# Kernel tuning notes

Measured on AMD Instinct MI355X. Metric: run time of the kernel, lower is better.

Reference implementation:

```python
import jax, jax.numpy as jnp
import numpy as np

N_U = 20000; N_I = 20000; D = 256
NNZ = 600000; EGG = 300000; EDD = 300000; B = 8192
DROP = 0.1; LAM2 = 1e-7


def _attention(x, W, a, edges):
    # GAT-style attention over sampled relationship edges (src -> tgt).
    n, d = x.shape
    h = x @ W                                  # [n, d]
    src, tgt = edges[0], edges[1]
    e = jax.nn.leaky_relu((h @ a[:d])[src] + (h @ a[d:])[tgt], 0.2)  # [E]
    m = jax.ops.segment_max(e, tgt, num_segments=n)
    m = jnp.where(jnp.isfinite(m), m, 0.0)
    ex = jnp.exp(e - m[tgt])
    denom = jax.ops.segment_sum(ex, tgt, num_segments=n)             # [n]
    num = jax.ops.segment_sum(ex[:, None] * h[src], tgt, num_segments=n)  # [n, d]
    return num / (denom[:, None] + 1e-9)


def _spmm(rows, cols, vals, x, n_out):
    # sparse [n_out, n_in] @ dense [n_in, d]
    return jax.ops.segment_sum(vals[:, None] * x[cols], rows, num_segments=n_out)


def _mlp(x, W1, b1, W2, b2, W3, b3):
    h = jax.nn.relu(x @ W1 + b1)
    h = jax.nn.relu(h @ W2 + b2)
    return (h @ W3 + b3)[..., 0]


def setup_inputs() -> dict:
    key = jax.random.key(0)
    ks = jax.random.split(key, 24)
    s = 0.02
    inp = {
        'E_g_0': jax.random.normal(ks[0], (N_U, D), jnp.float32) * s,
        'E_d_0': jax.random.normal(ks[1], (N_I, D), jnp.float32) * s,
        'att_W': jax.random.normal(ks[2], (D, D), jnp.float32) * s,
        'att_a': jax.random.normal(ks[3], (2 * D,), jnp.float32) * s,
        'att1_W': jax.random.normal(ks[4], (D, D), jnp.float32) * s,
        'att1_a': jax.random.normal(ks[5], (2 * D,), jnp.float32) * s,
        'W1': jax.random.normal(ks[6], (2 * D, D), jnp.float32) * s,
        'b1': jnp.zeros((D,), jnp.float32),
        'W2': jax.random.normal(ks[7], (D, D), jnp.float32) * s,
        'b2': jnp.zeros((D,), jnp.float32),
        'W3': jax.random.normal(ks[8], (D, 1), jnp.float32) * s,
        'b3': jnp.zeros((1,), jnp.float32),
        'M1': jax.random.normal(ks[9], (2 * D, D), jnp.float32) * s,
        'mb1': jnp.zeros((D,), jnp.float32),
        'M2': jax.random.normal(ks[10], (D, D), jnp.float32) * s,
        'mb2': jnp.zeros((D,), jnp.float32),
        'adj_vals': jax.random.uniform(ks[11], (NNZ,), jnp.float32),
        'uids': jax.random.randint(ks[12], (B,), 0, N_U, jnp.int32),
        'iids': jax.random.randint(ks[13], (B,), 0, N_I, jnp.int32),
        'pos': jax.random.randint(ks[14], (B,), 0, N_I, jnp.int32),
        'neg': jax.random.randint(ks[15], (B,), 0, N_I, jnp.int32),
        'gene_edges': jax.random.randint(ks[16], (2, EGG), 0, N_U, jnp.int32),
        'drug_edges': jax.random.randint(ks[17], (2, EDD), 0, N_I, jnp.int32),
        'adj_rows': jax.random.randint(ks[18], (NNZ,), 0, N_U, jnp.int32),
        'adj_cols': jax.random.randint(ks[19], (NNZ,), 0, N_I, jnp.int32),
        'drop1': jax.random.bernoulli(ks[20], 1.0 - DROP, (NNZ,)),
        'drop2': jax.random.bernoulli(ks[21], 1.0 - DROP, (NNZ,)),
    }
    return inp


def reference(E_g_0, E_d_0, att_W, att_a, att1_W, att1_a, W1, b1, W2, b2, W3, b3,
              M1, mb1, M2, mb2, adj_vals, uids, iids, pos, neg,
              gene_edges, drug_edges, adj_rows, adj_cols, drop1, drop2):
    # Attention-modulated layer-0 embeddings
    E_d0 = 0.1 * _attention(E_d_0, att_W, att_a, drug_edges) + E_d_0
    E_g0 = 0.1 * _attention(E_g_0, att_W, att_a, gene_edges) + E_g_0

    # sparse_dropout + spmm (two independent dropout draws, as in the source)
    scale = 1.0 / (1.0 - DROP)
    v1 = adj_vals * drop1.astype(adj_vals.dtype) * scale
    v2 = adj_vals * drop2.astype(adj_vals.dtype) * scale
    E_g = _spmm(adj_rows, adj_cols, v1, E_d0, N_U)   # adj @ E_d0
    E_d = _spmm(adj_cols, adj_rows, v2, E_g0, N_I)   # adj.T @ E_g0

    u = E_g[uids]; p = E_d[pos]; ng = E_d[neg]
    pos_s = _mlp(jnp.concatenate([u, p], axis=-1), W1, b1, W2, b2, W3, b3)
    neg_s = _mlp(jnp.concatenate([u, ng], axis=-1), W1, b1, W2, b2, W3, b3)

    # BCE-with-logits (labels 1 for pos, 0 for neg) + BPR term
    loss_pos = jnp.mean(jax.nn.softplus(-pos_s))
    loss_neg = jnp.mean(jax.nn.softplus(neg_s))
    loss_bpr = jnp.mean(jax.nn.softplus(-(pos_s - neg_s)))
    loss_r = loss_pos + loss_neg + loss_bpr

    params = (E_g_0, E_d_0, att_W, att_a, att1_W, att1_a,
              W1, b1, W2, b2, W3, b3, M1, mb1, M2, mb2)
    loss_reg = LAM2 * sum(jnp.sum(p_ * p_) for p_ in params)

    loss = loss_reg + loss_r  # loss_s == 0
    return jnp.stack([loss, loss_r, jnp.zeros((), loss.dtype)])
```

## Files before the change

kernel.cpp:

```cpp
#include <hip/hip_runtime.h>
#include <math.h>

#define N_NODES 20000
#define D       256
#define NNZ     600000
#define NEDGE   300000
#define BATCH   8192
#define DROP_SCALE (1.0f/0.9f)
#define LAM2_F  1e-7f

#define M_PAD   20096
#define CSTRIDE 20032

#define C_ATT 56
#define C_ADJ 80

#define BINW 320
#define NBIN 63
#define TILE_E 2048
#define EPT 8
#define T_ATT ((NEDGE + TILE_E - 1) / TILE_E)
#define T_ADJ ((NNZ + TILE_E - 1) / TILE_E)
#define NBLK_P1 (2 * T_ATT + 2 * T_ADJ)
#define CAP_BIN_ATT 5376
#define CAP_BIN_ADJ 6144

#define FP8_SCALE 256.0f
#define VSCALE    58980.0f
#define INV_VSCALE (1.0f/58980.0f)

typedef unsigned short u16;
typedef unsigned char  u8;
typedef __attribute__((ext_vector_type(8))) short bf16x8;
typedef __attribute__((ext_vector_type(4))) float f32x4;
typedef __attribute__((ext_vector_type(2))) float f32x2;
typedef __attribute__((ext_vector_type(4))) u16   v4h;
typedef __attribute__((ext_vector_type(4))) unsigned v4u;

__device__ inline float wave_reduce(float v) {
    #pragma unroll
    for (int off = 32; off > 0; off >>= 1) v += __shfl_down(v, off, 64);
    return v;
}

__device__ inline float softplus_f(float x) {
    float r = log1pf(__expf(-fabsf(x)));
    return x > 0.f ? x + r : r;
}

__device__ inline u16 f2bf(float f) {
    unsigned u = __float_as_uint(f);
    unsigned r = u + 0x7fff + ((u >> 16) & 1);
    return (u16)(r >> 16);
}
__device__ inline float bf2f(u16 b) { return __uint_as_float(((unsigned)b) << 16); }

__device__ inline unsigned f32x4_to_fp8x4(float a, float b, float c, float d) {
    int r = 0;
    r = __builtin_amdgcn_cvt_pk_fp8_f32(a, b, r, false);
    r = __builtin_amdgcn_cvt_pk_fp8_f32(c, d, r, true);
    return (unsigned)r;
}
__device__ inline u8 f32_to_fp8(float a) {
    int r = __builtin_amdgcn_cvt_pk_fp8_f32(a, a, 0, false);
    return (u8)(r & 0xff);
}

__device__ inline void gld_lds16(const void* g, void* l) {
    __builtin_amdgcn_global_load_lds((const __attribute__((address_space(1))) void*)g,
                                     (__attribute__((address_space(3))) void*)l, 16, 0, 0);
}

__global__ __launch_bounds__(256) void init_kernel(const unsigned char* __restrict__ drop,
                                                   const int* __restrict__ uids, const int* __restrict__ pos,
                                                   const int* __restrict__ neg,
                                                   const float* __restrict__ att_W, const float* __restrict__ att_a,
                                                   float* __restrict__ wlv, float* __restrict__ wrv,
                                                   unsigned* __restrict__ bm2, unsigned* __restrict__ bm3,
                                                   unsigned int* __restrict__ flag) {
    if (blockIdx.x < 96) {
        int i = blockIdx.x * blockDim.x + threadIdx.x;
        if (i < BATCH) {
            int v = uids[i];
            atomicOr(&bm2[v >> 5], 1u << (v & 31));
        } else if (i < 2 * BATCH) {
            int v = pos[i - BATCH];
            atomicOr(&bm3[v >> 5], 1u << (v & 31));
        } else {
            int v = neg[i - 2 * BATCH];
            atomicOr(&bm3[v >> 5], 1u << (v & 31));
        }
    } else if (blockIdx.x == 96) {
        __shared__ int cnt_s;
        if (threadIdx.x == 0) cnt_s = 0;
        __syncthreads();
        int c = 0;
        for (int i = threadIdx.x; i < 1024; i += blockDim.x)
            if (drop[4*i + 1] != 0) c++;
        atomicAdd(&cnt_s, c);
        __syncthreads();
        if (threadIdx.x == 0) *flag = (cnt_s > 64) ? 1u : 0u;
    } else {
        int t = threadIdx.x;
        float s1 = 0.f, s2 = 0.f;
        for (int n = 0; n < D; n++) {
            float w = att_W[(size_t)t * D + n];
            s1 += w * att_a[n];
            s2 += w * att_a[D + n];
        }
        wlv[t] = s1; wrv[t] = s2;
    }
}

__global__ __launch_bounds__(256) void p1_kernel(
        const int* __restrict__ dtgt, const int* __restrict__ dsrc,
        const int* __restrict__ gtgt, const int* __restrict__ gsrc,
        const int* __restrict__ ar,   const int* __restrict__ ac,
        const float* __restrict__ vals,
        const void* __restrict__ drop1, const void* __restrict__ drop2,
        const unsigned int* __restrict__ flag,
        const unsigned* __restrict__ bm2, const unsigned* __restrict__ bm3,
        int* __restrict__ pcur, unsigned* __restrict__ attbin, uint2* __restrict__ adjbin) {
    __shared__ int hist[NBIN];
    __shared__ int basep[NBIN];
    for (int i = threadIdx.x; i < NBIN; i += 256) hist[i] = 0;
    __syncthreads();

    int b = blockIdx.x;
    int s, t0;
    if (b < T_ATT)               { s = 0; t0 = b; }
    else if (b < 2 * T_ATT)      { s = 1; t0 = b - T_ATT; }
    else if (b < 2*T_ATT + T_ADJ){ s = 2; t0 = b - 2 * T_ATT; }
    else                         { s = 3; t0 = b - 2 * T_ATT - T_ADJ; }
    int base = t0 * TILE_E;
    int regN = (s < 2) ? NEDGE : NNZ;

    int bins[EPT], rank[EPT];
    unsigned key[EPT], pay[EPT];
    float pv[EPT];

    if (s < 2) {
        const int* tgt = (s == 0) ? dtgt : gtgt;
        const int* src = (s == 0) ? dsrc : gsrc;
        #pragma unroll
        for (int e = 0; e < EPT; e++) {
            int idx = base + e * 256 + threadIdx.x;
            rank[e] = -1;
            if (idx < regN) {
                int k = __builtin_nontemporal_load(tgt + idx);
                int sv = __builtin_nontemporal_load(src + idx);
                key[e] = (unsigned)k; pay[e] = (unsigned)sv;
                bins[e] = k / BINW;
                rank[e] = atomicAdd(&hist[bins[e]], 1);
            }
        }
    } else {
        const unsigned int bf = *flag;
        const int* keyp = (s == 2) ? ar : ac;
        const int* othp = (s == 2) ? ac : ar;
        const void* drp = (s == 2) ? drop1 : drop2;
        const unsigned* bm = (s == 2) ? bm2 : bm3;
        #pragma unroll
        for (int e = 0; e < EPT; e++) {
            int idx = base + e * 256 + threadIdx.x;
            rank[e] = -1;
            if (idx < regN) {
                int k = __builtin_nontemporal_load(keyp + idx);
                if ((bm[k >> 5] >> (k & 31)) & 1) {
                    bool keep = bf ? (__builtin_nontemporal_load((const u8*)drp + idx) != 0)
                                   : (__builtin_nontemporal_load((const unsigned*)drp + idx) != 0);
                    if (keep) {
                        float v = __builtin_nontemporal_load(vals + idx) * DROP_SCALE;
                        int oth = __builtin_nontemporal_load(othp + idx);
                        key[e] = (unsigned)k; pay[e] = (unsigned)oth; pv[e] = v;
                        bins[e] = k / BINW;
                        rank[e] = atomicAdd(&hist[bins[e]], 1);
                    }
                }
            }
        }
    }
    __syncthreads();
    for (int i = threadIdx.x; i < NBIN; i += 256) {
        int h = hist[i];
        basep[i] = h ? atomicAdd(&pcur[s * NBIN + i], h) : 0;
    }
    __syncthreads();
    if (s < 2) {
        unsigned* seg = attbin + (size_t)s * NBIN * CAP_BIN_ATT;
        #pragma unroll
        for (int e = 0; e < EPT; e++) {
            if (rank[e] < 0) continue;
            int pos = basep[bins[e]] + rank[e];
            if (pos < CAP_BIN_ATT)
                seg[(size_t)bins[e] * CAP_BIN_ATT + pos] = key[e] | (pay[e] << 16);
        }
    } else {
        uint2* seg = adjbin + (size_t)(s - 2) * NBIN * CAP_BIN_ADJ;
        #pragma unroll
        for (int e = 0; e < EPT; e++) {
            if (rank[e] < 0) continue;
            int pos = basep[bins[e]] + rank[e];
            if (pos < CAP_BIN_ADJ) {
                uint2 pr; pr.x = key[e] | (pay[e] << 16); pr.y = __float_as_uint(pv[e]);
                seg[(size_t)bins[e] * CAP_BIN_ADJ + pos] = pr;
            }
        }
    }
}

__global__ __launch_bounds__(1024) void p2_kernel(
        const int* __restrict__ pcur, const unsigned* __restrict__ attbin,
        const uint2* __restrict__ adjbin,
        int* __restrict__ cnt, u16* __restrict__ srcs, unsigned* __restrict__ adj) {
    int s   = blockIdx.x / NBIN;
    int bin = blockIdx.x - s * NBIN;
    int nodeBase = bin * BINW;
    __shared__ int cur[BINW];
    for (int t = threadIdx.x; t < BINW; t += blockDim.x) cur[t] = 0;
    __syncthreads();
    if (s < 2) {
        int m = pcur[s * NBIN + bin]; if (m > CAP_BIN_ATT) m = CAP_BIN_ATT;
        const unsigned* seg = attbin + ((size_t)s * NBIN + bin) * CAP_BIN_ATT;
        for (int k = threadIdx.x; k < m; k += blockDim.x) {
            unsigned e = seg[k];
            int lk = (int)(e & 0xFFFFu) - nodeBase;
            int c = atomicAdd(&cur[lk], 1);
            if (c < C_ATT)
                srcs[(size_t)s * N_NODES * C_ATT + (size_t)(nodeBase + lk) * C_ATT + c] = (u16)(e >> 16);
        }
        __syncthreads();
        for (int t = threadIdx.x; t < BINW; t += blockDim.x) {
            int node = nodeBase + t;
            if (node < N_NODES) {
                int n = cur[t]; if (n > C_ATT) n = C_ATT;
                cnt[s * CSTRIDE + node] = n;
            }
        }
    } else {
        int m = pcur[s * NBIN + bin]; if (m > CAP_BIN_ADJ) m = CAP_BIN_ADJ;
        const uint2* seg = adjbin + ((size_t)(s - 2) * NBIN + bin) * CAP_BIN_ADJ;
        for (int k = threadIdx.x; k < m; k += blockDim.x) {
            uint2 e = seg[k];
            int lk  = (int)(e.x & 0xFFFFu) - nodeBase;
            int oth = (int)(e.x >> 16);
            float v = __uint_as_float(e.y);
            unsigned pk = ((unsigned)(v * VSCALE + 0.5f) << 16) | (unsigned)oth;
            int c = atomicAdd(&cur[lk], 1);
            if (c < C_ADJ)
                adj[(size_t)(s - 2) * N_NODES * C_ADJ + (size_t)(nodeBase + lk) * C_ADJ + c] = pk;
        }
        __syncthreads();
        for (int t = threadIdx.x; t < BINW; t += blockDim.x) {
            int node = nodeBase + t;
            if (node < N_NODES) {
                int n = cur[t]; if (n > C_ADJ) n = C_ADJ;
                cnt[s * CSTRIDE + node] = n;
            }
        }
    }
}

#define NB_CAST (2 * M_PAD / 4)
#define NB_T1   (D * D / 256)
#define NB_T2   (2 * D * D / 256)
#define NB_T3   (D * D / 256)
__global__ __launch_bounds__(256) void prep_kernel(
        const float* __restrict__ E_g, const float* __restrict__ E_d,
        u16* __restrict__ Eg_bf, u16* __restrict__ Ed_bf,
        const float* __restrict__ att_W,
        const float* __restrict__ W1, const float* __restrict__ W2,
        u16* __restrict__ attWT, u16* __restrict__ W1T, u16* __restrict__ W2T,
        const float* __restrict__ wlv, const float* __restrict__ wrv,
        float* __restrict__ hl_g, float* __restrict__ hr_g,
        float* __restrict__ hl_d, float* __restrict__ hr_d,
        float* __restrict__ regp) {
    int bid = blockIdx.x;
    if (bid < NB_CAST) {
        int wid  = (bid * 256 + threadIdx.x) >> 6;
        int lane = threadIdx.x & 63;
        int is_d = (wid >= M_PAD);
        int row  = is_d ? wid - M_PAD : wid;
        u16* dst = (is_d ? Ed_bf : Eg_bf) + (size_t)row * D;
        float s3 = 0.f;
        if (row >= N_NODES) {
            ((ushort4*)dst)[lane] = make_ushort4(0, 0, 0, 0);
        } else {
            const float* src = (is_d ? E_d : E_g) + (size_t)row * D;
            float4 e  = ((const float4*)src)[lane];
            float4 l4 = ((const float4*)wlv)[lane];
            float4 r4 = ((const float4*)wrv)[lane];
            ((ushort4*)dst)[lane] = make_ushort4(f2bf(e.x), f2bf(e.y), f2bf(e.z), f2bf(e.w));
            float s1 = e.x*l4.x + e.y*l4.y + e.z*l4.z + e.w*l4.w;
            float s2 = e.x*r4.x + e.y*r4.y + e.z*r4.z + e.w*r4.w;
            s3 = e.x*e.x + e.y*e.y + e.z*e.z + e.w*e.w;
            s1 = wave_reduce(s1); s2 = wave_reduce(s2);
            if (lane == 0) {
                if (is_d) { hl_d[row] = s1; hr_d[row] = s2; }
                else      { hl_g[row] = s1; hr_g[row] = s2; }
            }
        }
        s3 = wave_reduce(s3);
        __shared__ float sm3[4];
        if (lane == 0) sm3[threadIdx.x >> 6] = s3;
        __syncthreads();
        if (threadIdx.x == 0) regp[bid] = sm3[0] + sm3[1] + sm3[2] + sm3[3];
    } else if (bid < NB_CAST + NB_T1) {
        int o = (bid - NB_CAST) * 256 + threadIdx.x;
        int n = o >> 8, k = o & 255;
        attWT[o] = f2bf(att_W[(size_t)k * D + n]);
    } else if (bid < NB_CAST + NB_T1 + NB_T2) {
        int o = (bid - NB_CAST - NB_T1) * 256 + threadIdx.x;
        int n = o / (2 * D), k = o - n * (2 * D);
        W1T[o] = f2bf(W1[(size_t)k * D + n]);
    } else {
        int o = (bid - NB_CAST - NB_T1 - NB_T2) * 256 + threadIdx.x;
        int n = o >> 8, k = o & 255;
        W2T[o] = f2bf(W2[(size_t)k * D + n]);
    }
}

__global__ __launch_bounds__(256) void gemm_bf16(const u16* __restrict__ A_, const u16* __restrict__ BT,
                                                 void* __restrict__ C_, int M, int N, int K,
                                                 const float* __restrict__ bias, int do_relu, int out_mode,
                                                 const u16* __restrict__ A2, void* __restrict__ C2) {
    const u16* A = A_; void* C = C_;
    if (A2 && blockIdx.z == 1) { A = A2; C = C2; }
    __shared__ __align__(16) short As[128][32];
    __shared__ __align__(16) short Bs[128][32];
    int tid = threadIdx.x;
    int wave = tid >> 6, lane = tid & 63;
    int bm = blockIdx.x * 128, bn = blockIdx.y * 128;
    int sr = lane >> 2;
    int sc = (lane & 3) * 8;

    f32x4 acc[4][4];
    #pragma unroll
    for (int i = 0; i < 4; i++)
        #pragma unroll
        for (int j = 0; j < 4; j++)
            #pragma unroll
            for (int r = 0; r < 4; r++) acc[i][j][r] = 0.f;

    int wr = (wave >> 1) * 64;
    int wc = (wave & 1) * 64;
    int fr = lane & 15;
    int fk = (lane >> 4) * 8;

    for (int k0 = 0; k0 < K; k0 += 32) {
        #pragma unroll
        for (int j = 0; j < 2; j++) {
            int r0 = wave * 32 + j * 16;
            gld_lds16(A  + (size_t)(bm + r0 + sr) * K + k0 + sc, &As[r0][0]);
            gld_lds16(BT + (size_t)(bn + r0 + sr) * K + k0 + sc, &Bs[r0][0]);
        }
        __syncthreads();
        bf16x8 af[4], bfr[4];
        #pragma unroll
        for (int i = 0; i < 4; i++) af[i]  = *(const bf16x8*)&As[wr + i*16 + fr][fk];
        #pragma unroll
        for (int j = 0; j < 4; j++) bfr[j] = *(const bf16x8*)&Bs[wc + j*16 + fr][fk];
        #pragma unroll
        for (int i = 0; i < 4; i++)
            #pragma unroll
            for (int j = 0; j < 4; j++)
                acc[i][j] = __builtin_amdgcn_mfma_f32_16x16x32_bf16(af[i], bfr[j], acc[i][j], 0, 0, 0);
        __syncthreads();
    }

    #pragma unroll
    for (int j = 0; j < 4; j++) {
        int col = bn + wc + j * 16 + fr;
        float bv = (bias && out_mode == 0) ? bias[col] : 0.f;
        #pragma unroll
        for (int i = 0; i < 4; i++) {
            #pragma unroll
            for (int r = 0; r < 4; r++) {
                int row = bm + wr + i * 16 + (lane >> 4) * 4 + r;
                if (row < M) {
                    float v = acc[i][j][r] + bv;
                    if (out_mode == 0) {
                        if (do_relu) v = fmaxf(v, 0.f);
                        ((u16*)C)[(size_t)row * N + col] = f2bf(v);
                    } else {
                        ((u8*)C)[(size_t)row * N + col] = f32_to_fp8(v * FP8_SCALE);
                    }
                }
            }
        }
    }
}

__global__ __launch_bounds__(256) void att_kernel(const u8* __restrict__ h_d, const u8* __restrict__ h_g,
                                                  const float* __restrict__ hl_d, const float* __restrict__ hr_d,
                                                  const float* __restrict__ hl_g, const float* __restrict__ hr_g,
                                                  const int* __restrict__ cur, const u16* __restrict__ srcs,
                                                  const float* __restrict__ E_d_0, const float* __restrict__ E_g_0,
                                                  u8* __restrict__ E_d0p, u8* __restrict__ E_g0p) {
    int wid  = (blockIdx.x * blockDim.x + threadIdx.x) >> 6;
    int lane = threadIdx.x & 63;
    if (wid >= 2 * N_NODES) return;
    int is_g = (wid >= N_NODES);
    int node = is_g ? wid - N_NODES : wid;
    const u8* h     = is_g ? h_g : h_d;
    const float* hl = is_g ? hl_g : hl_d;
    float hrn       = (is_g ? hr_g : hr_d)[node];
    int reg         = is_g ? 1 : 0;
    const u16* sv   = srcs + (size_t)reg * N_NODES * C_ATT + (size_t)node * C_ATT;
    int n = cur[reg * CSTRIDE + node];
    if (n > C_ATT) n = C_ATT;
    float ax = 0.f, ay = 0.f, az = 0.f, aw = 0.f, denom = 0.f;
    int k = 0;
    for (; k + 4 <= n; k += 4) {
        v4h s4 = __builtin_nontemporal_load((const v4h*)(sv + k));
        int s0 = s4[0], s1 = s4[1], s2 = s4[2], s3 = s4[3];
        float l0 = hl[s0], l1 = hl[s1], l2 = hl[s2], l3 = hl[s3];
        unsigned g0 = ((const unsigned*)(h + (size_t)s0 * D))[lane];
        unsigned g1 = ((const unsigned*)(h + (size_t)s1 * D))[lane];
        unsigned g2 = ((const unsigned*)(h + (size_t)s2 * D))[lane];
        unsigned g3 = ((const unsigned*)(h + (size_t)s3 * D))[lane];
        float e0 = l0 + hrn; e0 = e0 > 0.f ? e0 : 0.2f * e0; float x0 = __expf(e0);
        float e1 = l1 + hrn; e1 = e1 > 0.f ? e1 : 0.2f * e1; float x1 = __expf(e1);
        float e2 = l2 + hrn; e2 = e2 > 0.f ? e2 : 0.2f * e2; float x2 = __expf(e2);
        float e3 = l3 + hrn; e3 = e3 > 0.f ? e3 : 0.2f * e3; float x3 = __expf(e3);
        denom += x0 + x1 + x2 + x3;
        f32x2 lo, hi;
        lo = __builtin_amdgcn_cvt_pk_f32_fp8(g0, false); hi = __builtin_amdgcn_cvt_pk_f32_fp8(g0, true);
        ax += x0*lo[0]; ay += x0*lo[1]; az += x0*hi[0]; aw += x0*hi[1];
        lo = __builtin_amdgcn_cvt_pk_f32_fp8(g1, false); hi = __builtin_amdgcn_cvt_pk_f32_fp8(g1, true);
        ax += x1*lo[0]; ay += x1*lo[1]; az += x1*hi[0]; aw += x1*hi[1];
        lo = __builtin_amdgcn_cvt_pk_f32_fp8(g2, false); hi = __builtin_amdgcn_cvt_pk_f32_fp8(g2, true);
        ax += x2*lo[0]; ay += x2*lo[1]; az += x2*hi[0]; aw += x2*hi[1];
        lo = __builtin_amdgcn_cvt_pk_f32_fp8(g3, false); hi = __builtin_amdgcn_cvt_pk_f32_fp8(g3, true);
        ax += x3*lo[0]; ay += x3*lo[1]; az += x3*hi[0]; aw += x3*hi[1];
    }
    for (; k < n; k++) {
        int s = sv[k];
        float ev = hl[s] + hrn;
        ev = ev > 0.f ? ev : 0.2f * ev;
        float ex = __expf(ev);
        denom += ex;
        unsigned g = ((const unsigned*)(h + (size_t)s * D))[lane];
        f32x2 lo = __builtin_amdgcn_cvt_pk_f32_fp8(g, false);
        f32x2 hi = __builtin_amdgcn_cvt_pk_f32_fp8(g, true);
        ax += ex*lo[0]; ay += ex*lo[1]; az += ex*hi[0]; aw += ex*hi[1];
    }
    float sc = 0.1f / (denom + 1e-9f);
    const float* E0 = is_g ? E_g_0 : E_d_0;
    u8*         out = is_g ? E_g0p : E_d0p;
    float4 b = ((const float4*)(E0 + (size_t)node * D))[lane];
    unsigned pk = f32x4_to_fp8x4(FP8_SCALE * b.x + sc * ax, FP8_SCALE * b.y + sc * ay,
                                 FP8_SCALE * b.z + sc * az, FP8_SCALE * b.w + sc * aw);
    ((unsigned*)(out + (size_t)node * D))[lane] = pk;
}

__global__ __launch_bounds__(256) void pull_kernel(const int* __restrict__ uids, const int* __restrict__ pos,
                                                   const int* __restrict__ neg,
                                                   const int* __restrict__ cur, const unsigned* __restrict__ adj,
                                                   const u8* __restrict__ E_d0p, const u8* __restrict__ E_g0p,
                                                   u16* __restrict__ X) {
    int wid  = (blockIdx.x * blockDim.x + threadIdx.x) >> 6;
    int lane = threadIdx.x & 63;
    if (wid >= 3 * BATCH) return;
    int type = wid >> 13;
    int b    = wid & (BATCH - 1);
    int node, reg; const u8* E;
    if (type == 0)      { node = uids[b]; reg = 2; E = E_d0p; }
    else if (type == 1) { node = pos[b];  reg = 3; E = E_g0p; }
    else                { node = neg[b];  reg = 3; E = E_g0p; }
    const unsigned* av = adj + (size_t)(reg - 2) * N_NODES * C_ADJ + (size_t)node * C_ADJ;
    int n = cur[reg * CSTRIDE + node];
    if (n > C_ADJ) n = C_ADJ;
    float ax = 0.f, ay = 0.f, az = 0.f, aw = 0.f;
    int k = 0;
    for (; k + 4 <= n; k += 4) {
        v4u q = __builtin_nontemporal_load((const v4u*)(av + k));
        int c0 = q[0] & 0xFFFF, c1 = q[1] & 0xFFFF, c2 = q[2] & 0xFFFF, c3 = q[3] & 0xFFFF;
        float v0 = (float)(q[0] >> 16) * INV_VSCALE, v1 = (float)(q[1] >> 16) * INV_VSCALE;
        float v2 = (float)(q[2] >> 16) * INV_VSCALE, v3 = (float)(q[3] >> 16) * INV_VSCALE;
        unsigned g0 = ((const unsigned*)(E + (size_t)c0 * D))[lane];
        unsigned g1 = ((const unsigned*)(E + (size_t)c1 * D))[lane];
        unsigned g2 = ((const unsigned*)(E + (size_t)c2 * D))[lane];
        unsigned g3 = ((const unsigned*)(E + (size_t)c3 * D))[lane];
        f32x2 lo, hi;
        lo = __builtin_amdgcn_cvt_pk_f32_fp8(g0, false); hi = __builtin_amdgcn_cvt_pk_f32_fp8(g0, true);
        ax += v0*lo[0]; ay += v0*lo[1]; az += v0*hi[0]; aw += v0*hi[1];
        lo = __builtin_amdgcn_cvt_pk_f32_fp8(g1, false); hi = __builtin_amdgcn_cvt_pk_f32_fp8(g1, true);
        ax += v1*lo[0]; ay += v1*lo[1]; az += v1*hi[0]; aw += v1*hi[1];
        lo = __builtin_amdgcn_cvt_pk_f32_fp8(g2, false); hi = __builtin_amdgcn_cvt_pk_f32_fp8(g2, true);
        ax += v2*lo[0]; ay += v2*lo[1]; az += v2*hi[0]; aw += v2*hi[1];
        lo = __builtin_amdgcn_cvt_pk_f32_fp8(g3, false); hi = __builtin_amdgcn_cvt_pk_f32_fp8(g3, true);
        ax += v3*lo[0]; ay += v3*lo[1]; az += v3*hi[0]; aw += v3*hi[1];
    }
    for (; k < n; k++) {
        unsigned q = av[k];
        int c = q & 0xFFFF;
        float v = (float)(q >> 16) * INV_VSCALE;
        unsigned g = ((const unsigned*)(E + (size_t)c * D))[lane];
        f32x2 lo = __builtin_amdgcn_cvt_pk_f32_fp8(g, false);
        f32x2 hi = __builtin_amdgcn_cvt_pk_f32_fp8(g, true);
        ax += v*lo[0]; ay += v*lo[1]; az += v*hi[0]; aw += v*hi[1];
    }
    const float inv = 1.0f / FP8_SCALE;
    ushort4 r = make_ushort4(f2bf(ax * inv), f2bf(ay * inv), f2bf(az * inv), f2bf(aw * inv));
    if (type == 0) {
        ((ushort4*)(X + (size_t)b * 2 * D))[lane] = r;
        ((ushort4*)(X + (size_t)(BATCH + b) * 2 * D))[lane] = r;
    } else if (type == 1) {
        ((ushort4*)(X + (size_t)b * 2 * D + D))[lane] = r;
    } else {
        ((ushort4*)(X + (size_t)(BATCH + b) * 2 * D + D))[lane] = r;
    }
}

__global__ __launch_bounds__(256) void score_kernel(const u16* __restrict__ H2, const float* __restrict__ W3,
                                                    const float* __restrict__ b3, float* __restrict__ s) {
    int wid  = (blockIdx.x * blockDim.x + threadIdx.x) >> 6;
    int lane = threadIdx.x & 63;
    if (wid >= 2 * BATCH) return;
    ushort4 hv = ((const ushort4*)(H2 + (size_t)wid * D))[lane];
    float4 w  = ((const float4*)W3)[lane];
    float d = bf2f(hv.x) * w.x + bf2f(hv.y) * w.y + bf2f(hv.z) * w.z + bf2f(hv.w) * w.w;
    d = wave_reduce(d);
    if (lane == 0) s[wid] = d + b3[0];
}

__global__ __launch_bounds__(256) void loss_kernel(const float* __restrict__ s, float* __restrict__ acc) {
    float lp = 0.f, ln = 0.f, lb = 0.f;
    for (int i = blockIdx.x * blockDim.x + threadIdx.x; i < BATCH; i += gridDim.x * blockDim.x) {
        float ps = s[i], ns = s[BATCH + i];
        lp += softplus_f(-ps);
        ln += softplus_f(ns);
        lb += softplus_f(-(ps - ns));
    }
    lp = wave_reduce(lp); ln = wave_reduce(ln); lb = wave_reduce(lb);
    __shared__ float sm[3][4];
    int w = threadIdx.x >> 6, lane = threadIdx.x & 63;
    if (lane == 0) { sm[0][w] = lp; sm[1][w] = ln; sm[2][w] = lb; }
    __syncthreads();
    if (threadIdx.x == 0) {
        float a = 0.f, b = 0.f, c = 0.f;
        for (int i = 0; i < 4; i++) { a += sm[0][i]; b += sm[1][i]; c += sm[2][i]; }
        atomicAdd(&acc[1], a); atomicAdd(&acc[2], b); atomicAdd(&acc[3], c);
    }
}

struct RegArgs { const float* p[14]; int n[14]; };

__global__ __launch_bounds__(256) void reg_kernel(RegArgs ra, float* __restrict__ acc) {
    const float* p = ra.p[blockIdx.x];
    int n = ra.n[blockIdx.x];
    int base = blockIdx.y * 4096;
    if (base >= n) return;
    float sum = 0.f;
    if (base + 4096 <= n) {
        const float4* p4 = (const float4*)(p + base);
        float4 v = p4[threadIdx.x];
        sum += v.x*v.x + v.y*v.y + v.z*v.z + v.w*v.w;
        v = p4[256 + threadIdx.x];
        sum += v.x*v.x + v.y*v.y + v.z*v.z + v.w*v.w;
        v = p4[512 + threadIdx.x];
        sum += v.x*v.x + v.y*v.y + v.z*v.z + v.w*v.w;
        v = p4[768 + threadIdx.x];
        sum += v.x*v.x + v.y*v.y + v.z*v.z + v.w*v.w;
    } else {
        int end = n;
        for (int i = base + threadIdx.x; i < end; i += 256) { float v = p[i]; sum += v * v; }
    }
    sum = wave_reduce(sum);
    __shared__ float sm[4];
    int w = threadIdx.x >> 6, lane = threadIdx.x & 63;
    if (lane == 0) sm[w] = sum;
    __syncthreads();
    if (threadIdx.x == 0) atomicAdd(&acc[0], sm[0] + sm[1] + sm[2] + sm[3]);
}

__global__ __launch_bounds__(256) void final_kernel(const float* __restrict__ acc,
                                                    const float* __restrict__ regp,
                                                    float* __restrict__ out) {
    float sum = 0.f;
    for (int i = threadIdx.x; i < NB_CAST; i += 256) sum += regp[i];
    sum = wave_reduce(sum);
    __shared__ float sm[4];
    int w = threadIdx.x >> 6, lane = threadIdx.x & 63;
    if (lane == 0) sm[w] = sum;
    __syncthreads();
    if (threadIdx.x == 0) {
        float reg = acc[0] + sm[0] + sm[1] + sm[2] + sm[3];
        float lr = (acc[1] + acc[2] + acc[3]) * (1.0f / (float)BATCH);
        out[0] = LAM2_F * reg + lr;
        out[1] = lr;
        out[2] = 0.f;
    }
}

extern "C" void kernel_launch(void* const* d_in, const int* in_sizes, int n_in,
                              void* d_out, int out_size, void* d_ws, size_t ws_size,
                              hipStream_t stream) {
    (void)n_in; (void)out_size; (void)ws_size;
    const float* E_g_0   = (const float*)d_in[0];
    const float* E_d_0   = (const float*)d_in[1];
    const float* att_W   = (const float*)d_in[2];
    const float* att_a   = (const float*)d_in[3];
    const float* W1      = (const float*)d_in[6];
    const float* b1      = (const float*)d_in[7];
    const float* W2      = (const float*)d_in[8];
    const float* b2      = (const float*)d_in[9];
    const float* W3      = (const float*)d_in[10];
    const float* b3      = (const float*)d_in[11];
    const float* adj_vals= (const float*)d_in[16];
    const int*   uids    = (const int*)d_in[17];
    const int*   pos     = (const int*)d_in[19];
    const int*   neg     = (const int*)d_in[20];
    const int*   gene_e  = (const int*)d_in[21];
    const int*   drug_e  = (const int*)d_in[22];
    const int*   adj_rows= (const int*)d_in[23];
    const int*   adj_cols= (const int*)d_in[24];
    const void*  drop1   = d_in[25];
    const void*  drop2   = d_in[26];

    char* ws = (char*)d_ws;
    size_t cur_off = 0;
    auto take = [&](size_t bytes) -> void* {
        void* p = ws + cur_off;
        cur_off += (bytes + 255) & ~(size_t)255;
        return p;
    };
    u16* Eg_bf = (u16*)take((size_t)M_PAD * D * 2);
    u16* Ed_bf = (u16*)take((size_t)M_PAD * D * 2);
    u16* X     = Eg_bf;
    u16* attWT = (u16*)take((size_t)D * D * 2);
    u16* W1T   = (u16*)take((size_t)D * 2 * D * 2);
    u16* W2T   = (u16*)take((size_t)D * D * 2);
    u8*  h_g   = (u8*)take((size_t)M_PAD * D);
    u8*  h_d   = (u8*)take((size_t)M_PAD * D);
    u8*  E_g0p = (u8*)take((size_t)N_NODES * D);
    u8*  E_d0p = (u8*)take((size_t)N_NODES * D);
    u16* H1    = (u16*)take((size_t)2 * BATCH * D * 2);
    u16* H2    = (u16*)take((size_t)2 * BATCH * D * 2);
    float* hl_g = (float*)take((size_t)N_NODES * 4);
    float* hr_g = (float*)take((size_t)N_NODES * 4);
    float* hl_d = (float*)take((size_t)N_NODES * 4);
    float* hr_d = (float*)take((size_t)N_NODES * 4);
    float* wlv  = (float*)take((size_t)D * 4);
    float* wrv  = (float*)take((size_t)D * 4);
    float* sbuf = (float*)take((size_t)2 * BATCH * 4);
    float* regp = (float*)take((size_t)NB_CAST * 4);
    u16*   srcs = (u16*)take((size_t)2 * N_NODES * C_ATT * 2);
    unsigned* adj = (unsigned*)take((size_t)2 * N_NODES * C_ADJ * 4);
    int*   cnt  = (int*)take((size_t)4 * CSTRIDE * 4);
    unsigned* attbin = (unsigned*)take((size_t)2 * NBIN * CAP_BIN_ATT * 4);
    uint2*    adjbin = (uint2*)take((size_t)2 * NBIN * CAP_BIN_ADJ * 8);
    int*      pcur = (int*)take((size_t)4 * NBIN * 4);
    unsigned* bm2  = (unsigned*)take(4096);
    unsigned* bm3  = (unsigned*)take(4096);
    float*    acc  = (float*)take(256);
    size_t zbytes = (char*)(acc + 64) - (char*)pcur;

    hipMemsetAsync(pcur, 0, zbytes, stream);
    init_kernel<<<98, 256, 0, stream>>>((const unsigned char*)drop1, uids, pos, neg,
                                        att_W, att_a, wlv, wrv,
                                        bm2, bm3, (unsigned int*)(acc + 4));

    p1_kernel<<<NBLK_P1, 256, 0, stream>>>(drug_e + NEDGE, drug_e, gene_e + NEDGE, gene_e,
                                           adj_rows, adj_cols, adj_vals, drop1, drop2,
                                           (const unsigned int*)(acc + 4), bm2, bm3,
                                           pcur, attbin, adjbin);
    p2_kernel<<<4 * NBIN, 1024, 0, stream>>>(pcur, attbin, adjbin, cnt, srcs, adj);

    prep_kernel<<<NB_CAST + NB_T1 + NB_T2 + NB_T3, 256, 0, stream>>>(
        E_g_0, E_d_0, Eg_bf, Ed_bf, att_W, W1, W2,
        attWT, W1T, W2T, wlv, wrv, hl_g, hr_g, hl_d, hr_d, regp);

    gemm_bf16<<<dim3(M_PAD / 128, 2, 2), 256, 0, stream>>>(Eg_bf, attWT, h_g, N_NODES, D, D,
                                                           nullptr, 0, 1, Ed_bf, h_d);
    att_kernel<<<10000, 256, 0, stream>>>(h_d, h_g, hl_d, hr_d, hl_g, hr_g,
                                          cnt, srcs, E_d_0, E_g_0, E_d0p, E_g0p);

    pull_kernel<<<6144, 256, 0, stream>>>(uids, pos, neg, cnt, adj, E_d0p, E_g0p, X);

    gemm_bf16<<<dim3(2 * BATCH / 128, 2, 1), 256, 0, stream>>>(X,  W1T, H1, 2 * BATCH, D, 2 * D,
                                                               b1, 1, 0, nullptr, nullptr);
    gemm_bf16<<<dim3(2 * BATCH / 128, 2, 1), 256, 0, stream>>>(H1, W2T, H2, 2 * BATCH, D, D,
                                                               b2, 1, 0, nullptr, nullptr);
    score_kernel<<<4096, 256, 0, stream>>>(H2, W3, b3, sbuf);

    loss_kernel<<<16, 256, 0, stream>>>(sbuf, acc);
    RegArgs ra;
    for (int i = 0; i < 14; i++) { ra.p[i] = (const float*)d_in[i + 2]; ra.n[i] = in_sizes[i + 2]; }
    reg_kernel<<<dim3(14, 32), 256, 0, stream>>>(ra, acc);
    final_kernel<<<1, 256, 0, stream>>>(acc, regp, (float*)d_out);
}
```

Measured before the change: 352.4 us.

## Precompute attention edge weights in bucketing pass and unroll gathers by eight

The p2 bucketing kernel now runs after prep and computes each edge's exp(leaky_relu(hl[src]+hr[tgt])) once, packing it as fp16 next to the 16-bit source index. The attention kernel then streams the packed pairs instead of doing random hl lookups and exps per edge, and reads the residual from the bf16 copy instead of fp32. Both the attention and pull kernels unroll their gather loops to eight independent row loads for more memory-level parallelism. The cost is a doubled srcs buffer, fp16 rounding of the weights, and bf16 rounding of the residual term.

```diff
diff --git a/kernel.cpp b/kernel.cpp
--- a/kernel.cpp
+++ b/kernel.cpp
@@ -54,6 +54,14 @@
     return (u16)(r >> 16);
 }
 __device__ inline float bf2f(u16 b) { return __uint_as_float(((unsigned)b) << 16); }
+
+__device__ inline u16 f2h(float f) {
+    _Float16 h = (_Float16)f;
+    return __builtin_bit_cast(u16, h);
+}
+__device__ inline float h2f(u16 b) {
+    return (float)__builtin_bit_cast(_Float16, b);
+}
 
 __device__ inline unsigned f32x4_to_fp8x4(float a, float b, float c, float d) {
     int r = 0;
@@ -212,7 +220,9 @@
 __global__ __launch_bounds__(1024) void p2_kernel(
         const int* __restrict__ pcur, const unsigned* __restrict__ attbin,
         const uint2* __restrict__ adjbin,
-        int* __restrict__ cnt, u16* __restrict__ srcs, unsigned* __restrict__ adj) {
+        const float* __restrict__ hl_d, const float* __restrict__ hr_d,
+        const float* __restrict__ hl_g, const float* __restrict__ hr_g,
+        int* __restrict__ cnt, unsigned* __restrict__ srcs, unsigned* __restrict__ adj) {
     int s   = blockIdx.x / NBIN;
     int bin = blockIdx.x - s * NBIN;
     int nodeBase = bin * BINW;
@@ -222,12 +232,19 @@
     if (s < 2) {
         int m = pcur[s * NBIN + bin]; if (m > CAP_BIN_ATT) m = CAP_BIN_ATT;
         const unsigned* seg = attbin + ((size_t)s * NBIN + bin) * CAP_BIN_ATT;
+        const float* hl = (s == 0) ? hl_d : hl_g;
+        const float* hr = (s == 0) ? hr_d : hr_g;
         for (int k = threadIdx.x; k < m; k += blockDim.x) {
             unsigned e = seg[k];
-            int lk = (int)(e & 0xFFFFu) - nodeBase;
+            int lk  = (int)(e & 0xFFFFu) - nodeBase;
+            int src = (int)(e >> 16);
+            float ev = hl[src] + hr[nodeBase + lk];
+            ev = ev > 0.f ? ev : 0.2f * ev;
+            u16 xh = f2h(__expf(ev));
             int c = atomicAdd(&cur[lk], 1);
             if (c < C_ATT)
-                srcs[(size_t)s * N_NODES * C_ATT + (size_t)(nodeBase + lk) * C_ATT + c] = (u16)(e >> 16);
+                srcs[(size_t)s * N_NODES * C_ATT + (size_t)(nodeBase + lk) * C_ATT + c] =
+                    (unsigned)src | ((unsigned)xh << 16);
         }
         __syncthreads();
         for (int t = threadIdx.x; t < BINW; t += blockDim.x) {
@@ -392,65 +409,71 @@
 }
 
 __global__ __launch_bounds__(256) void att_kernel(const u8* __restrict__ h_d, const u8* __restrict__ h_g,
-                                                  const float* __restrict__ hl_d, const float* __restrict__ hr_d,
-                                                  const float* __restrict__ hl_g, const float* __restrict__ hr_g,
-                                                  const int* __restrict__ cur, const u16* __restrict__ srcs,
-                                                  const float* __restrict__ E_d_0, const float* __restrict__ E_g_0,
+                                                  const int* __restrict__ cur, const unsigned* __restrict__ srcs,
+                                                  const u16* __restrict__ Ed_bf, const u16* __restrict__ Eg_bf,
                                                   u8* __restrict__ E_d0p, u8* __restrict__ E_g0p) {
     int wid  = (blockIdx.x * blockDim.x + threadIdx.x) >> 6;
     int lane = threadIdx.x & 63;
     if (wid >= 2 * N_NODES) return;
     int is_g = (wid >= N_NODES);
     int node = is_g ? wid - N_NODES : wid;
-    const u8* h     = is_g ? h_g : h_d;
-    const float* hl = is_g ? hl_g : hl_d;
-    float hrn       = (is_g ? hr_g : hr_d)[node];
-    int reg         = is_g ? 1 : 0;
-    const u16* sv   = srcs + (size_t)reg * N_NODES * C_ATT + (size_t)node * C_ATT;
+    const unsigned* h32 = (const unsigned*)(is_g ? h_g : h_d);
+    int reg = is_g ? 1 : 0;
+    const unsigned* sv = srcs + (size_t)reg * N_NODES * C_ATT + (size_t)node * C_ATT;
     int n = cur[reg * CSTRIDE + node];
     if (n > C_ATT) n = C_ATT;
     float ax = 0.f, ay = 0.f, az = 0.f, aw = 0.f, denom = 0.f;
     int k = 0;
+    for (; k + 8 <= n; k += 8) {
+        v4u qa = __builtin_nontemporal_load((const v4u*)(sv + k));
+        v4u qb = __builtin_nontemporal_load((const v4u*)(sv + k + 4));
+        unsigned g[8]; float x[8];
+        #pragma unroll
+        for (int j = 0; j < 4; j++) {
+            g[j]     = h32[((size_t)(qa[j] & 0xFFFFu) << 6) + lane];
+            g[4 + j] = h32[((size_t)(qb[j] & 0xFFFFu) << 6) + lane];
+            x[j]     = h2f((u16)(qa[j] >> 16));
+            x[4 + j] = h2f((u16)(qb[j] >> 16));
+        }
+        #pragma unroll
+        for (int j = 0; j < 8; j++) {
+            denom += x[j];
+            f32x2 lo = __builtin_amdgcn_cvt_pk_f32_fp8(g[j], false);
+            f32x2 hi = __builtin_amdgcn_cvt_pk_f32_fp8(g[j], true);
+            ax += x[j]*lo[0]; ay += x[j]*lo[1]; az += x[j]*hi[0]; aw += x[j]*hi[1];
+        }
+    }
     for (; k + 4 <= n; k += 4) {
-        v4h s4 = __builtin_nontemporal_load((const v4h*)(sv + k));
-        int s0 = s4[0], s1 = s4[1], s2 = s4[2], s3 = s4[3];
-        float l0 = hl[s0], l1 = hl[s1], l2 = hl[s2], l3 = hl[s3];
-        unsigned g0 = ((const unsigned*)(h + (size_t)s0 * D))[lane];
-        unsigned g1 = ((const unsigned*)(h + (size_t)s1 * D))[lane];
-        unsigned g2 = ((const unsigned*)(h + (size_t)s2 * D))[lane];
-        unsigned g3 = ((const unsigned*)(h + (size_t)s3 * D))[lane];
-        float e0 = l0 + hrn; e0 = e0 > 0.f ? e0 : 0.2f * e0; float x0 = __expf(e0);
-        float e1 = l1 + hrn; e1 = e1 > 0.f ? e1 : 0.2f * e1; float x1 = __expf(e1);
-        float e2 = l2 + hrn; e2 = e2 > 0.f ? e2 : 0.2f * e2; float x2 = __expf(e2);
-        float e3 = l3 + hrn; e3 = e3 > 0.f ? e3 : 0.2f * e3; float x3 = __expf(e3);
-        denom += x0 + x1 + x2 + x3;
-        f32x2 lo, hi;
-        lo = __builtin_amdgcn_cvt_pk_f32_fp8(g0, false); hi = __builtin_amdgcn_cvt_pk_f32_fp8(g0, true);
-        ax += x0*lo[0]; ay += x0*lo[1]; az += x0*hi[0]; aw += x0*hi[1];
-        lo = __builtin_amdgcn_cvt_pk_f32_fp8(g1, false); hi = __builtin_amdgcn_cvt_pk_f32_fp8(g1, true);
-        ax += x1*lo[0]; ay += x1*lo[1]; az += x1*hi[0]; aw += x1*hi[1];
-        lo = __builtin_amdgcn_cvt_pk_f32_fp8(g2, false); hi = __builtin_amdgcn_cvt_pk_f32_fp8(g2, true);
-        ax += x2*lo[0]; ay += x2*lo[1]; az += x2*hi[0]; aw += x2*hi[1];
-        lo = __builtin_amdgcn_cvt_pk_f32_fp8(g3, false); hi = __builtin_amdgcn_cvt_pk_f32_fp8(g3, true);
-        ax += x3*lo[0]; ay += x3*lo[1]; az += x3*hi[0]; aw += x3*hi[1];
+        v4u qa = __builtin_nontemporal_load((const v4u*)(sv + k));
+        unsigned g[4]; float x[4];
+        #pragma unroll
+        for (int j = 0; j < 4; j++) {
+            g[j] = h32[((size_t)(qa[j] & 0xFFFFu) << 6) + lane];
+            x[j] = h2f((u16)(qa[j] >> 16));
+        }
+        #pragma unroll
+        for (int j = 0; j < 4; j++) {
+            denom += x[j];
+            f32x2 lo = __builtin_amdgcn_cvt_pk_f32_fp8(g[j], false);
+            f32x2 hi = __builtin_amdgcn_cvt_pk_f32_fp8(g[j], true);
+            ax += x[j]*lo[0]; ay += x[j]*lo[1]; az += x[j]*hi[0]; aw += x[j]*hi[1];
+        }
     }
     for (; k < n; k++) {
-        int s = sv[k];
-        float ev = hl[s] + hrn;
-        ev = ev > 0.f ? ev : 0.2f * ev;
-        float ex = __expf(ev);
-        denom += ex;
-        unsigned g = ((const unsigned*)(h + (size_t)s * D))[lane];
+        unsigned q = sv[k];
+        float xv = h2f((u16)(q >> 16));
+        unsigned g = h32[((size_t)(q & 0xFFFFu) << 6) + lane];
+        denom += xv;
         f32x2 lo = __builtin_amdgcn_cvt_pk_f32_fp8(g, false);
         f32x2 hi = __builtin_amdgcn_cvt_pk_f32_fp8(g, true);
-        ax += ex*lo[0]; ay += ex*lo[1]; az += ex*hi[0]; aw += ex*hi[1];
+        ax += xv*lo[0]; ay += xv*lo[1]; az += xv*hi[0]; aw += xv*hi[1];
     }
     float sc = 0.1f / (denom + 1e-9f);
-    const float* E0 = is_g ? E_g_0 : E_d_0;
-    u8*         out = is_g ? E_g0p : E_d0p;
-    float4 b = ((const float4*)(E0 + (size_t)node * D))[lane];
-    unsigned pk = f32x4_to_fp8x4(FP8_SCALE * b.x + sc * ax, FP8_SCALE * b.y + sc * ay,
-                                 FP8_SCALE * b.z + sc * az, FP8_SCALE * b.w + sc * aw);
+    const u16* E0b = is_g ? Eg_bf : Ed_bf;
+    u8*       out  = is_g ? E_g0p : E_d0p;
+    ushort4 b4 = ((const ushort4*)(E0b + (size_t)node * D))[lane];
+    unsigned pk = f32x4_to_fp8x4(FP8_SCALE * bf2f(b4.x) + sc * ax, FP8_SCALE * bf2f(b4.y) + sc * ay,
+                                 FP8_SCALE * bf2f(b4.z) + sc * az, FP8_SCALE * bf2f(b4.w) + sc * aw);
     ((unsigned*)(out + (size_t)node * D))[lane] = pk;
 }
 
@@ -468,35 +491,50 @@
     if (type == 0)      { node = uids[b]; reg = 2; E = E_d0p; }
     else if (type == 1) { node = pos[b];  reg = 3; E = E_g0p; }
     else                { node = neg[b];  reg = 3; E = E_g0p; }
+    const unsigned* E32 = (const unsigned*)E;
     const unsigned* av = adj + (size_t)(reg - 2) * N_NODES * C_ADJ + (size_t)node * C_ADJ;
     int n = cur[reg * CSTRIDE + node];
     if (n > C_ADJ) n = C_ADJ;
     float ax = 0.f, ay = 0.f, az = 0.f, aw = 0.f;
     int k = 0;
+    for (; k + 8 <= n; k += 8) {
+        v4u qa = __builtin_nontemporal_load((const v4u*)(av + k));
+        v4u qb = __builtin_nontemporal_load((const v4u*)(av + k + 4));
+        unsigned g[8]; float v[8];
+        #pragma unroll
+        for (int j = 0; j < 4; j++) {
+            g[j]     = E32[((size_t)(qa[j] & 0xFFFFu) << 6) + lane];
+            g[4 + j] = E32[((size_t)(qb[j] & 0xFFFFu) << 6) + lane];
+            v[j]     = (float)(qa[j] >> 16) * INV_VSCALE;
+            v[4 + j] = (float)(qb[j] >> 16) * INV_VSCALE;
+        }
+        #pragma unroll
+        for (int j = 0; j < 8; j++) {
+            f32x2 lo = __builtin_amdgcn_cvt_pk_f32_fp8(g[j], false);
+            f32x2 hi = __builtin_amdgcn_cvt_pk_f32_fp8(g[j], true);
+            ax += v[j]*lo[0]; ay += v[j]*lo[1]; az += v[j]*hi[0]; aw += v[j]*hi[1];
+        }
+    }
     for (; k + 4 <= n; k += 4) {
-        v4u q = __builtin_nontemporal_load((const v4u*)(av + k));
-        int c0 = q[0] & 0xFFFF, c1 = q[1] & 0xFFFF, c2 = q[2] & 0xFFFF, c3 = q[3] & 0xFFFF;
-        float v0 = (float)(q[0] >> 16) * INV_VSCALE, v1 = (float)(q[1] >> 16) * INV_VSCALE;
-        float v2 = (float)(q[2] >> 16) * INV_VSCALE, v3 = (float)(q[3] >> 16) * INV_VSCALE;
-        unsigned g0 = ((const unsigned*)(E + (size_t)c0 * D))[lane];
-        unsigned g1 = ((const unsigned*)(E + (size_t)c1 * D))[lane];
-        unsigned g2 = ((const unsigned*)(E + (size_t)c2 * D))[lane];
-        unsigned g3 = ((const unsigned*)(E + (size_t)c3 * D))[lane];
-        f32x2 lo, hi;
-        lo = __builtin_amdgcn_cvt_pk_f32_fp8(g0, false); hi = __builtin_amdgcn_cvt_pk_f32_fp8(g0, true);
-        ax += v0*lo[0]; ay += v0*lo[1]; az += v0*hi[0]; aw += v0*hi[1];
-        lo = __builtin_amdgcn_cvt_pk_f32_fp8(g1, false); hi = __builtin_amdgcn_cvt_pk_f32_fp8(g1, true);
-        ax += v1*lo[0]; ay += v1*lo[1]; az += v1*hi[0]; aw += v1*hi[1];
-        lo = __builtin_amdgcn_cvt_pk_f32_fp8(g2, false); hi = __builtin_amdgcn_cvt_pk_f32_fp8(g2, true);
-        ax += v2*lo[0]; ay += v2*lo[1]; az += v2*hi[0]; aw += v2*hi[1];
-        lo = __builtin_amdgcn_cvt_pk_f32_fp8(g3, false); hi = __builtin_amdgcn_cvt_pk_f32_fp8(g3, true);
-        ax += v3*lo[0]; ay += v3*lo[1]; az += v3*hi[0]; aw += v3*hi[1];
+        v4u qa = __builtin_nontemporal_load((const v4u*)(av + k));
+        unsigned g[4]; float v[4];
+        #pragma unroll
+        for (int j = 0; j < 4; j++) {
+            g[j] = E32[((size_t)(qa[j] & 0xFFFFu) << 6) + lane];
+            v[j] = (float)(qa[j] >> 16) * INV_VSCALE;
+        }
+        #pragma unroll
+        for (int j = 0; j < 4; j++) {
+            f32x2 lo = __builtin_amdgcn_cvt_pk_f32_fp8(g[j], false);
+            f32x2 hi = __builtin_amdgcn_cvt_pk_f32_fp8(g[j], true);
+            ax += v[j]*lo[0]; ay += v[j]*lo[1]; az += v[j]*hi[0]; aw += v[j]*hi[1];
+        }
     }
     for (; k < n; k++) {
         unsigned q = av[k];
         int c = q & 0xFFFF;
         float v = (float)(q >> 16) * INV_VSCALE;
-        unsigned g = ((const unsigned*)(E + (size_t)c * D))[lane];
+        unsigned g = E32[((size_t)c << 6) + lane];
         f32x2 lo = __builtin_amdgcn_cvt_pk_f32_fp8(g, false);
         f32x2 hi = __builtin_amdgcn_cvt_pk_f32_fp8(g, true);
         ax += v*lo[0]; ay += v*lo[1]; az += v*hi[0]; aw += v*hi[1];
@@ -646,8 +684,8 @@
     float* wrv  = (float*)take((size_t)D * 4);
     float* sbuf = (float*)take((size_t)2 * BATCH * 4);
     float* regp = (float*)take((size_t)NB_CAST * 4);
-    u16*   srcs = (u16*)take((size_t)2 * N_NODES * C_ATT * 2);
-    unsigned* adj = (unsigned*)take((size_t)2 * N_NODES * C_ADJ * 4);
+    unsigned* srcs = (unsigned*)take((size_t)2 * N_NODES * C_ATT * 4);
+    unsigned* adj  = (unsigned*)take((size_t)2 * N_NODES * C_ADJ * 4);
     int*   cnt  = (int*)take((size_t)4 * CSTRIDE * 4);
     unsigned* attbin = (unsigned*)take((size_t)2 * NBIN * CAP_BIN_ATT * 4);
     uint2*    adjbin = (uint2*)take((size_t)2 * NBIN * CAP_BIN_ADJ * 8);
@@ -666,16 +704,18 @@
                                            adj_rows, adj_cols, adj_vals, drop1, drop2,
                                            (const unsigned int*)(acc + 4), bm2, bm3,
                                            pcur, attbin, adjbin);
-    p2_kernel<<<4 * NBIN, 1024, 0, stream>>>(pcur, attbin, adjbin, cnt, srcs, adj);
 
     prep_kernel<<<NB_CAST + NB_T1 + NB_T2 + NB_T3, 256, 0, stream>>>(
         E_g_0, E_d_0, Eg_bf, Ed_bf, att_W, W1, W2,
         attWT, W1T, W2T, wlv, wrv, hl_g, hr_g, hl_d, hr_d, regp);
 
+    p2_kernel<<<4 * NBIN, 1024, 0, stream>>>(pcur, attbin, adjbin,
+                                             hl_d, hr_d, hl_g, hr_g, cnt, srcs, adj);
+
     gemm_bf16<<<dim3(M_PAD / 128, 2, 2), 256, 0, stream>>>(Eg_bf, attWT, h_g, N_NODES, D, D,
                                                            nullptr, 0, 1, Ed_bf, h_d);
-    att_kernel<<<10000, 256, 0, stream>>>(h_d, h_g, hl_d, hr_d, hl_g, hr_g,
-                                          cnt, srcs, E_d_0, E_g_0, E_d0p, E_g0p);
+    att_kernel<<<10000, 256, 0, stream>>>(h_d, h_g, cnt, srcs,
+                                          Ed_bf, Eg_bf, E_d0p, E_g0p);
 
     pull_kernel<<<6144, 256, 0, stream>>>(uids, pos, neg, cnt, adj, E_d0p, E_g0p, X);
 
```

Result: faster. 341.2 us (-3.2%).
